# Performance work log

Measured on AMD Instinct MI355X. Metric: run time of the kernel, lower is better.

Reference implementation:

```python
import jax, jax.numpy as jnp
import numpy as np

NEG_SLOPE = 0.01  # torch F.leaky_relu default

def _lrelu(x):
    return jax.nn.leaky_relu(x, NEG_SLOPE)

def setup_inputs() -> dict:
    key = jax.random.key(0)
    ks = jax.random.split(key, 24)
    B, N, E = 512, 20000, 640000
    n_enc_1, n_enc_2, n_z = 512, 256, 64
    n_dec_2, n_dec_1, hidden = 256, 512, 256
    p = lambda k, shp, fan: jax.random.normal(k, shp, jnp.float32) * (1.0 / np.sqrt(fan))
    return {
        "data": jax.random.normal(ks[0], (B, N), jnp.float32),
        "noise": jax.random.normal(ks[1], (B, N), jnp.float32),
        "edge_index": jax.random.randint(ks[2], (2, E), 0, N, jnp.int32),
        "w_gcn": jax.random.normal(ks[3], (), jnp.float32),
        "b_gcn": jax.random.normal(ks[4], (), jnp.float32) * 0.1,
        "enc1_w": p(ks[5], (N, n_enc_1), N), "enc1_b": p(ks[6], (n_enc_1,), N),
        "enc2_w": p(ks[7], (n_enc_1, n_enc_2), n_enc_1), "enc2_b": p(ks[8], (n_enc_2,), n_enc_1),
        "enc3_w": p(ks[9], (n_enc_2, n_z), n_enc_2), "enc3_b": p(ks[10], (n_z,), n_enc_2),
        "dec1_w": p(ks[11], (n_z, n_dec_2), n_z), "dec1_b": p(ks[12], (n_dec_2,), n_z),
        "dec2_w": p(ks[13], (n_dec_2, n_dec_1), n_dec_2), "dec2_b": p(ks[14], (n_dec_1,), n_dec_2),
        "dec3_w": p(ks[15], (n_dec_1, N), n_dec_1), "dec3_b": p(ks[16], (N,), n_dec_1),
        "disc1_w": p(ks[17], (n_z, hidden), n_z), "disc1_b": p(ks[18], (hidden,), n_z),
        "disc2_w": p(ks[19], (hidden, hidden), hidden), "disc2_b": p(ks[20], (hidden,), hidden),
        "disc3_w": p(ks[21], (hidden, 1), hidden), "disc3_b": p(ks[22], (1,), hidden),
    }

def _gcn_batched(x, edge_index, w_gcn, b_gcn):
    # x: [B, N] -> GCNConv(1,1, improved=True) applied per row, vectorized.
    B, N = x.shape
    src, dst = edge_index[0], edge_index[1]
    loop = jnp.arange(N, dtype=src.dtype)
    src_a = jnp.concatenate([src, loop])
    dst_a = jnp.concatenate([dst, loop])
    # improved=True: self-loop edge weight 2.0
    ew = jnp.concatenate([jnp.ones(src.shape[0], x.dtype), jnp.full((N,), 2.0, x.dtype)])
    deg = jax.ops.segment_sum(ew, dst_a, num_segments=N)
    dinv = jnp.where(deg > 0, jax.lax.rsqrt(deg), 0.0)
    norm = dinv[src_a] * ew * dinv[dst_a]  # [E+N]
    xl = x * w_gcn                         # lin (1x1 weight, no bias)
    msgs = xl[:, src_a] * norm[None, :]    # [B, E+N]
    agg = jnp.zeros_like(x).at[:, dst_a].add(msgs)
    return agg + b_gcn

def reference(data, noise, edge_index, w_gcn, b_gcn,
              enc1_w, enc1_b, enc2_w, enc2_b, enc3_w, enc3_b,
              dec1_w, dec1_b, dec2_w, dec2_b, dec3_w, dec3_b,
              disc1_w, disc1_b, disc2_w, disc2_b, disc3_w, disc3_b):
    x = data + noise * 0.1
    gcn_out = _lrelu(_gcn_batched(x, edge_index, w_gcn, b_gcn))  # [B, N]
    h1 = _lrelu(gcn_out @ enc1_w + enc1_b)
    h2 = _lrelu(h1 @ enc2_w + enc2_b)
    z = _lrelu(h2 @ enc3_w + enc3_b)
    d1 = _lrelu(z @ dec1_w + dec1_b)
    d2 = _lrelu(d1 @ dec2_w + dec2_b)
    dec_h3 = _lrelu(d2 @ dec3_w + dec3_b)
    g1 = _lrelu(z @ disc1_w + disc1_b)
    g2 = _lrelu(g1 @ disc2_w + disc2_b)
    d = jax.nn.sigmoid(g2 @ disc3_w + disc3_b)
    return (dec_h3, z, d)
```

## Files before the change

kernel.cpp:

```cpp
#include <hip/hip_runtime.h>
#include <hip/hip_bf16.h>


#define LRELU(v) ((v) > 0.f ? (v) : 0.01f * (v))

static constexpr int Bb = 512;
static constexpr int Nn = 20000;
static constexpr int Ee = 640000;
static constexpr int KBn = 2500;
static constexpr int NPD = 20096;

typedef __attribute__((ext_vector_type(8))) short short8;
typedef __attribute__((ext_vector_type(4))) float f32x4;

__device__ __forceinline__ ushort f2bf(float f) {
  uint u = __builtin_bit_cast(uint, f);
  u = u + 0x7FFFu + ((u >> 16) & 1u);
  return (ushort)(u >> 16);
}
__device__ __forceinline__ float bfLo(uint u) {
  return __builtin_bit_cast(float, u << 16);
}
__device__ __forceinline__ float bfHi(uint u) {
  return __builtin_bit_cast(float, u & 0xffff0000u);
}

__global__ void transpose_xs_k(const float* __restrict__ a, const float* __restrict__ nz,
                               const float* __restrict__ dinv, ushort* __restrict__ xs) {
  __shared__ ushort tile[64][65];
  int c0 = blockIdx.x * 64;
  int p = blockIdx.y;
  int chunk = p >> 1;
  int sub = (p & 1) * 64;
  int rbase = p * 64;
  for (int i = threadIdx.x; i < 64 * 64; i += 256) {
    int rr = i >> 6, cc = i & 63;
    int r = rbase + rr, c = c0 + cc;
    ushort v = 0;
    if (c < Nn) {
      size_t idx = (size_t)r * Nn + c;
      v = f2bf(dinv[c] * (a[idx] + 0.1f * nz[idx]));
    }
    tile[rr][cc] = v;
  }
  __syncthreads();
  for (int i = threadIdx.x; i < 64 * 64; i += 256) {
    int cc = i >> 6, rr = i & 63;
    int c = c0 + cc;
    if (c < Nn) xs[(size_t)chunk * Nn * 128 + (size_t)c * 128 + sub + rr] = tile[rr][cc];
  }
}

__global__ void hist_check_k(const int* __restrict__ src, const int* __restrict__ dst, int E,
                             int* __restrict__ cnt, int* __restrict__ flag) {
  int i = blockIdx.x * 256 + threadIdx.x;
  if (i < E) {
    int s = src[i], d = dst[i];
    if ((unsigned)s >= (unsigned)Nn || (unsigned)d >= (unsigned)Nn) {
      atomicExch(flag, 1);
    } else {
      atomicAdd(&cnt[d], 1);
    }
  }
}

__global__ void offs_k(const int* __restrict__ cnt, int* __restrict__ offs,
                       int* __restrict__ cursor, float* __restrict__ dinv,
                       int* __restrict__ bump) {
  int i = blockIdx.x * 256 + threadIdx.x;
  int l = threadIdx.x & 63;
  int v = (i < Nn) ? cnt[i] : 0;
  int x = v;
#pragma unroll
  for (int d = 1; d < 64; d <<= 1) {
    int t = __shfl_up(x, d);
    if (l >= d) x += t;
  }
  int total = __shfl(x, 63);
  int base = 0;
  if (l == 0) base = atomicAdd(bump, total);
  base = __shfl(base, 0);
  int excl = base + x - v;
  if (i < Nn) {
    offs[i] = excl;
    cursor[i] = excl;
    dinv[i] = rsqrtf(2.0f + (float)v);
  }
}

__global__ void scatter_k(const int* __restrict__ src, const int* __restrict__ dst, int E,
                          int* __restrict__ cursor, uint* __restrict__ eOff) {
  int i = blockIdx.x * 256 + threadIdx.x;
  if (i < E) {
    int s = src[i], d = dst[i];
    if ((unsigned)s >= (unsigned)Nn || (unsigned)d >= (unsigned)Nn) return;
    int p = atomicAdd(&cursor[d], 1);
    eOff[p] = (uint)s * 256u;
  }
}

__global__ __launch_bounds__(256) void spmm_fm_k(
    const ushort* __restrict__ xs, const uint* __restrict__ eOff, const int* __restrict__ offs,
    const int* __restrict__ cnt, const float* __restrict__ dinv, const float* __restrict__ wg,
    const float* __restrict__ bg, ushort* __restrict__ gfm) {
  __shared__ uint sIdx[4][64];
  __shared__ ushort sOut[128][8];
  int bid = blockIdx.x;
  int chunk = bid & 3;
  int grp = bid >> 2;
  int wv = threadIdx.x >> 6, l = threadIdx.x & 63;
  const char* base = (const char*)(xs + (size_t)chunk * Nn * 128) + l * 4;
  float wgv = wg[0], bb = bg[0];

#pragma unroll
  for (int sub = 0; sub < 2; ++sub) {
    int n = grp * 8 + wv * 2 + sub;
    int o = offs[n], c = cnt[n];
    const uint* ep = eOff + o;
    uint su = *(const uint*)(base + (size_t)n * 256);
    float a00 = 2.0f * bfLo(su), a01 = 2.0f * bfHi(su);
    float a10 = 0.f, a11 = 0.f;

    for (int bi = 0; bi < c; bi += 64) {
      int rem = c - bi;
      if (rem > 64) rem = 64;
      sIdx[wv][l] = (l < rem) ? ep[bi + l] : 0u;
      int i = 0;
      for (; i + 8 <= rem; i += 8) {
        uint u[8];
#pragma unroll
        for (int j = 0; j < 8; ++j) u[j] = *(const uint*)(base + sIdx[wv][i + j]);
#pragma unroll
        for (int j = 0; j < 8; j += 2) {
          a00 += bfLo(u[j]);
          a01 += bfHi(u[j]);
          a10 += bfLo(u[j + 1]);
          a11 += bfHi(u[j + 1]);
        }
      }
      for (; i < rem; ++i) {
        uint u = *(const uint*)(base + sIdx[wv][i]);
        a00 += bfLo(u);
        a01 += bfHi(u);
      }
    }

    float wdn = wgv * dinv[n];
    float v0 = wdn * (a00 + a10) + bb;
    float v1 = wdn * (a01 + a11) + bb;
    v0 = LRELU(v0);
    v1 = LRELU(v1);
    int j = wv * 2 + sub;
    sOut[2 * l][j] = f2bf(v0);
    sOut[2 * l + 1][j] = f2bf(v1);
  }
  __syncthreads();
  int row = threadIdx.x >> 1, half = threadIdx.x & 1;
  uint2 v = *(const uint2*)&sOut[row][half * 4];
  int m = chunk * 128 + row;
  *(uint2*)&gfm[((size_t)grp * 512 + m) * 8 + half * 4] = v;
}

__global__ void conv_we_k(const float* __restrict__ W, ushort* __restrict__ wef) {
  int n = blockIdx.x * 256 + threadIdx.x;
  int kb = blockIdx.y;
  ushort v[8];
#pragma unroll
  for (int j = 0; j < 8; ++j) v[j] = f2bf(W[(size_t)(8 * kb + j) * 512 + n]);
  uint4 pk;
  pk.x = (uint)v[0] | ((uint)v[1] << 16);
  pk.y = (uint)v[2] | ((uint)v[3] << 16);
  pk.z = (uint)v[4] | ((uint)v[5] << 16);
  pk.w = (uint)v[6] | ((uint)v[7] << 16);
  *(uint4*)&wef[((size_t)kb * 512 + n) * 8] = pk;
}

__global__ __launch_bounds__(256) void fmg_enc1_k(const ushort* __restrict__ gfm,
                                                  const ushort* __restrict__ wef,
                                                  float* __restrict__ C) {
  int n0 = blockIdx.x * 128, m0 = blockIdx.y * 128;
  int l = threadIdx.x & 63, w = threadIdx.x >> 6;
  int wr = w >> 1, wc = w & 1;
  int lrow = l & 15, lkg = l >> 4;
  f32x4 acc[4][4] = {};
  int ksBeg = blockIdx.z * 25, ksEnd = ksBeg + 25;

  for (int ks = ksBeg; ks < ksEnd; ++ks) {
    int kb = ks * 4 + lkg;
    short8 a[4], b[4];
#pragma unroll
    for (int mi = 0; mi < 4; ++mi) {
      int m = m0 + wr * 64 + mi * 16 + lrow;
      a[mi] = *(const short8*)&gfm[((size_t)kb * 512 + m) * 8];
    }
#pragma unroll
    for (int nj = 0; nj < 4; ++nj) {
      int n = n0 + wc * 64 + nj * 16 + lrow;
      b[nj] = *(const short8*)&wef[((size_t)kb * 512 + n) * 8];
    }
#pragma unroll
    for (int mi = 0; mi < 4; ++mi)
#pragma unroll
      for (int nj = 0; nj < 4; ++nj)
        acc[mi][nj] = __builtin_amdgcn_mfma_f32_16x16x32_bf16(a[mi], b[nj], acc[mi][nj], 0, 0, 0);
  }

#pragma unroll
  for (int mi = 0; mi < 4; ++mi)
#pragma unroll
    for (int nj = 0; nj < 4; ++nj)
#pragma unroll
      for (int r = 0; r < 4; ++r) {
        int row = m0 + wr * 64 + mi * 16 + lkg * 4 + r;
        int col = n0 + wc * 64 + nj * 16 + lrow;
        atomicAdd(&C[(size_t)row * 512 + col], acc[mi][nj][r]);
      }
}

__global__ void conv_wf_k(const float* __restrict__ W, ushort* __restrict__ wf) {
  int n = blockIdx.x * 256 + threadIdx.x;
  int kb = blockIdx.y;
  if (n >= NPD) return;
  ushort v[8];
#pragma unroll
  for (int j = 0; j < 8; ++j)
    v[j] = (n < Nn) ? f2bf(W[(size_t)(8 * kb + j) * Nn + n]) : (ushort)0;
  uint4 pk;
  pk.x = (uint)v[0] | ((uint)v[1] << 16);
  pk.y = (uint)v[2] | ((uint)v[3] << 16);
  pk.z = (uint)v[4] | ((uint)v[5] << 16);
  pk.w = (uint)v[6] | ((uint)v[7] << 16);
  *(uint4*)&wf[((size_t)kb * NPD + n) * 8] = pk;
}

__global__ __launch_bounds__(256) void fmg_dec3_k(const ushort* __restrict__ d2f,
                                                  const ushort* __restrict__ wf,
                                                  const float* __restrict__ bias,
                                                  float* __restrict__ C) {
  int n0 = blockIdx.x * 128, m0 = blockIdx.y * 128;
  int l = threadIdx.x & 63, w = threadIdx.x >> 6;
  int wr = w >> 1, wc = w & 1;
  int lrow = l & 15, lkg = l >> 4;
  f32x4 acc[4][4] = {};

#pragma unroll 4
  for (int ks = 0; ks < 16; ++ks) {
    int kb = ks * 4 + lkg;
    short8 a[4], b[4];
#pragma unroll
    for (int mi = 0; mi < 4; ++mi) {
      int m = m0 + wr * 64 + mi * 16 + lrow;
      a[mi] = *(const short8*)&d2f[((size_t)kb * 512 + m) * 8];
    }
#pragma unroll
    for (int nj = 0; nj < 4; ++nj) {
      int n = n0 + wc * 64 + nj * 16 + lrow;
      b[nj] = *(const short8*)&wf[((size_t)kb * NPD + n) * 8];
    }
#pragma unroll
    for (int mi = 0; mi < 4; ++mi)
#pragma unroll
      for (int nj = 0; nj < 4; ++nj)
        acc[mi][nj] = __builtin_amdgcn_mfma_f32_16x16x32_bf16(a[mi], b[nj], acc[mi][nj], 0, 0, 0);
  }

#pragma unroll
  for (int mi = 0; mi < 4; ++mi)
#pragma unroll
    for (int nj = 0; nj < 4; ++nj)
#pragma unroll
      for (int r = 0; r < 4; ++r) {
        int row = m0 + wr * 64 + mi * 16 + lkg * 4 + r;
        int col = n0 + wc * 64 + nj * 16 + lrow;
        if (col < Nn) {
          float v = acc[mi][nj][r] + bias[col];
          C[(size_t)row * Nn + col] = LRELU(v);
        }
      }
}

__global__ __launch_bounds__(256) void tail2_k(
    const float* __restrict__ h1, const float* __restrict__ c1, const float* __restrict__ W2,
    const float* __restrict__ c2, const float* __restrict__ W3, const float* __restrict__ c3,
    const float* __restrict__ Wd1, const float* __restrict__ cd1, const float* __restrict__ Wd2,
    const float* __restrict__ cd2, const float* __restrict__ Wg1, const float* __restrict__ cg1,
    const float* __restrict__ Wg2, const float* __restrict__ cg2, const float* __restrict__ Wg3,
    const float* __restrict__ cg3, float* __restrict__ out_z, float* __restrict__ out_d,
    ushort* __restrict__ d2f) {
  __shared__ float s_h1[512];
  __shared__ float s_h2[256];
  __shared__ float s_z[64];
  __shared__ float s_d1[256];
  __shared__ float s_g1[256];
  __shared__ float s_g2[256];
  __shared__ float s_part[4][256];
  __shared__ float s_red[4];
  int rl = blockIdx.x;
  int t = threadIdx.x;
  int w = t >> 6, l = t & 63;

  {
    float r0 = h1[(size_t)rl * 512 + t] + c1[t];
    float r1 = h1[(size_t)rl * 512 + t + 256] + c1[t + 256];
    s_h1[t] = LRELU(r0);
    s_h1[t + 256] = LRELU(r1);
  }
  __syncthreads();

  {
    int c4 = l * 4;
    float a0 = 0.f, a1 = 0.f, a2 = 0.f, a3 = 0.f;
#pragma unroll 8
    for (int k = w * 128; k < w * 128 + 128; ++k) {
      float4 wv = *(const float4*)&W2[(size_t)k * 256 + c4];
      float x = s_h1[k];
      a0 += x * wv.x; a1 += x * wv.y; a2 += x * wv.z; a3 += x * wv.w;
    }
    float4 pv = {a0, a1, a2, a3};
    *(float4*)&s_part[w][c4] = pv;
  }
  __syncthreads();
  s_h2[t] = LRELU(s_part[0][t] + s_part[1][t] + s_part[2][t] + s_part[3][t] + c2[t]);
  __syncthreads();

  {
    int c = t >> 2, p = t & 3;
    float a = 0.f;
#pragma unroll 8
    for (int k = p * 64; k < p * 64 + 64; ++k) a += s_h2[k] * W3[(size_t)k * 64 + c];
    s_part[p][c] = a;
  }
  __syncthreads();
  if (t < 64) {
    float v = s_part[0][t] + s_part[1][t] + s_part[2][t] + s_part[3][t] + c3[t];
    v = LRELU(v);
    s_z[t] = v;
    out_z[(size_t)rl * 64 + t] = v;
  }
  __syncthreads();

  {
    float a = 0.f;
#pragma unroll
    for (int k = 0; k < 64; ++k) a += s_z[k] * Wd1[(size_t)k * 256 + t];
    s_d1[t] = LRELU(a + cd1[t]);
  }
  {
    float a = 0.f;
#pragma unroll
    for (int k = 0; k < 64; ++k) a += s_z[k] * Wg1[(size_t)k * 256 + t];
    s_g1[t] = LRELU(a + cg1[t]);
  }
  __syncthreads();

  {
    int g = t & 127, p = t >> 7;
    int c4 = g * 4;
    float a0 = 0.f, a1 = 0.f, a2 = 0.f, a3 = 0.f;
#pragma unroll 8
    for (int k = p * 128; k < p * 128 + 128; ++k) {
      float4 wv = *(const float4*)&Wd2[(size_t)k * 512 + c4];
      float x = s_d1[k];
      a0 += x * wv.x; a1 += x * wv.y; a2 += x * wv.z; a3 += x * wv.w;
    }
    float* sp = &s_part[0][0];
    float4 pv = {a0, a1, a2, a3};
    *(float4*)&sp[p * 512 + c4] = pv;
  }
  __syncthreads();
  {
    const float* sp = &s_part[0][0];
#pragma unroll
    for (int cc = 0; cc < 2; ++cc) {
      int c = t + cc * 256;
      float v = sp[c] + sp[512 + c] + cd2[c];
      v = LRELU(v);
      d2f[((size_t)(c >> 3) * 512 + rl) * 8 + (c & 7)] = f2bf(v);
    }
  }
  __syncthreads();

  {
    int c4 = l * 4;
    float a0 = 0.f, a1 = 0.f, a2 = 0.f, a3 = 0.f;
#pragma unroll 8
    for (int k = w * 64; k < w * 64 + 64; ++k) {
      float4 wv = *(const float4*)&Wg2[(size_t)k * 256 + c4];
      float x = s_g1[k];
      a0 += x * wv.x; a1 += x * wv.y; a2 += x * wv.z; a3 += x * wv.w;
    }
    float4 pv = {a0, a1, a2, a3};
    *(float4*)&s_part[w][c4] = pv;
  }
  __syncthreads();
  s_g2[t] = LRELU(s_part[0][t] + s_part[1][t] + s_part[2][t] + s_part[3][t] + cg2[t]);
  __syncthreads();

  {
    float p = s_g2[t] * Wg3[t];
#pragma unroll
    for (int o = 32; o > 0; o >>= 1) p += __shfl_down(p, o);
    if ((t & 63) == 0) s_red[t >> 6] = p;
    __syncthreads();
    if (t == 0) {
      float s = s_red[0] + s_red[1] + s_red[2] + s_red[3] + cg3[0];
      out_d[rl] = 1.f / (1.f + __expf(-s));
    }
  }
}

__global__ void sentinel_k(float* out, float val) { out[0] = val; }
__global__ void flag_sentinel_k(float* out, const int* flag) {
  if (*flag != 0) out[0] = 70000.0f;
}

extern "C" void kernel_launch(void* const* d_in, const int* in_sizes, int n_in,
                              void* d_out, int out_size, void* d_ws, size_t ws_size,
                              hipStream_t stream) {
  const float* data = (const float*)d_in[0];
  const float* noise = (const float*)d_in[1];
  const int* edge = (const int*)d_in[2];
  const int* esrc_in = edge;
  const int* edst_in = edge + Ee;
  const float* w_gcn = (const float*)d_in[3];
  const float* b_gcn = (const float*)d_in[4];
  const float* enc1_w = (const float*)d_in[5];
  const float* enc1_b = (const float*)d_in[6];
  const float* enc2_w = (const float*)d_in[7];
  const float* enc2_b = (const float*)d_in[8];
  const float* enc3_w = (const float*)d_in[9];
  const float* enc3_b = (const float*)d_in[10];
  const float* dec1_w = (const float*)d_in[11];
  const float* dec1_b = (const float*)d_in[12];
  const float* dec2_w = (const float*)d_in[13];
  const float* dec2_b = (const float*)d_in[14];
  const float* dec3_w = (const float*)d_in[15];
  const float* dec3_b = (const float*)d_in[16];
  const float* disc1_w = (const float*)d_in[17];
  const float* disc1_b = (const float*)d_in[18];
  const float* disc2_w = (const float*)d_in[19];
  const float* disc2_b = (const float*)d_in[20];
  const float* disc3_w = (const float*)d_in[21];
  const float* disc3_b = (const float*)d_in[22];

  char* w = (char*)d_ws;
  size_t o = 0;
  auto alloc = [&](size_t bytes) {
    size_t r = o;
    o = (o + bytes + 15) & ~(size_t)15;
    return r;
  };
  size_t r1 = alloc((size_t)64 * NPD * 8 * 2);
  ushort* xs = (ushort*)(w + r1);
  ushort* wef = (ushort*)(w + r1);
  ushort* wf = (ushort*)(w + r1);
  ushort* gfm = (ushort*)(w + alloc((size_t)KBn * 512 * 8 * 2));
  float* h1 = (float*)(w + alloc(512 * 512 * 4));
  ushort* d2f = (ushort*)(w + alloc((size_t)64 * 512 * 8 * 2));
  float* dinv = (float*)(w + alloc(Nn * 4));
  int* cnt = (int*)(w + alloc(Nn * 4));
  int* offs = (int*)(w + alloc(Nn * 4));
  int* cursor = (int*)(w + alloc(Nn * 4));
  uint* eOff = (uint*)(w + alloc(Ee * 4));
  int* flag = (int*)(w + alloc(16));

  float* outp = (float*)d_out;
  float* out_dec = outp;
  float* out_z = outp + (size_t)Bb * Nn;
  float* out_d = out_z + (size_t)Bb * 64;

  static const int expect_sizes[23] = {
      10240000, 10240000, 1280000, 1, 1,
      10240000, 512, 131072, 256, 16384, 64,
      16384, 256, 131072, 512, 10240000, 20000,
      16384, 256, 65536, 256, 256, 1};
  float host_sentinel = 0.f;
  if (n_in != 23) host_sentinel = 50000.f;
  else if (out_size != 10273280) host_sentinel = 80000.f;
  else if (ws_size < 46100000u) host_sentinel = 60000.f;
  else {
    for (int i = 0; i < 23; ++i)
      if (in_sizes[i] != expect_sizes[i]) { host_sentinel = 100000.f + 1000.f * i; break; }
  }

  hipMemsetAsync(cnt, 0, Nn * sizeof(int), stream);
  hipMemsetAsync(flag, 0, 2 * sizeof(int), stream);
  hist_check_k<<<(Ee + 255) / 256, 256, 0, stream>>>(esrc_in, edst_in, Ee, cnt, flag);
  offs_k<<<(Nn + 255) / 256, 256, 0, stream>>>(cnt, offs, cursor, dinv, flag + 1);
  scatter_k<<<(Ee + 255) / 256, 256, 0, stream>>>(esrc_in, edst_in, Ee, cursor, eOff);

  {
    dim3 g((Nn + 63) / 64, 8);
    transpose_xs_k<<<g, 256, 0, stream>>>(data, noise, dinv, xs);
  }
  spmm_fm_k<<<(Nn / 8) * 4, 256, 0, stream>>>(xs, eOff, offs, cnt, dinv, w_gcn, b_gcn, gfm);
  {
    dim3 g(2, KBn);
    conv_we_k<<<g, 256, 0, stream>>>(enc1_w, wef);
  }
  hipMemsetAsync(h1, 0, 512 * 512 * 4, stream);
  {
    dim3 g(512 / 128, 512 / 128, 25);
    fmg_enc1_k<<<g, 256, 0, stream>>>(gfm, wef, h1);
  }
  tail2_k<<<Bb, 256, 0, stream>>>(h1, enc1_b, enc2_w, enc2_b, enc3_w, enc3_b, dec1_w, dec1_b,
                                  dec2_w, dec2_b, disc1_w, disc1_b, disc2_w, disc2_b, disc3_w,
                                  disc3_b, out_z, out_d, d2f);
  {
    dim3 g((NPD + 255) / 256, 64);
    conv_wf_k<<<g, 256, 0, stream>>>(dec3_w, wf);
  }
  {
    dim3 g(NPD / 128, 512 / 128);
    fmg_dec3_k<<<g, 256, 0, stream>>>(d2f, wf, dec3_b, out_dec);
  }

  flag_sentinel_k<<<1, 1, 0, stream>>>(out_dec, flag);
  if (host_sentinel != 0.f) sentinel_k<<<1, 1, 0, stream>>>(out_dec, host_sentinel);
}
```

Measured before the change: 288.9 us.

## Split tail MLP kernel into encoder and parallel decoder/discriminator kernels

Splits the per-row tail MLP into two kernels. One computes the encoder layers down to z and writes z to a workspace buffer. The second launches twice as many blocks so the decoder and discriminator branches run in parallel. The change also widens the SpMM gather unroll from 8 to 16 with a new 4-wide remainder loop, raises the tail loop unroll factors, and moves the h1 memset earlier. It adds a kernel launch and a small global round trip for z in exchange for more block-level parallelism.

```diff
diff --git a/kernel.cpp b/kernel.cpp
--- a/kernel.cpp
+++ b/kernel.cpp
@@ -126,17 +126,31 @@
       if (rem > 64) rem = 64;
       sIdx[wv][l] = (l < rem) ? ep[bi + l] : 0u;
       int i = 0;
-      for (; i + 8 <= rem; i += 8) {
-        uint u[8];
-#pragma unroll
-        for (int j = 0; j < 8; ++j) u[j] = *(const uint*)(base + sIdx[wv][i + j]);
-#pragma unroll
-        for (int j = 0; j < 8; j += 2) {
+      for (; i + 16 <= rem; i += 16) {
+        uint u[16];
+#pragma unroll
+        for (int j = 0; j < 16; ++j) u[j] = *(const uint*)(base + sIdx[wv][i + j]);
+#pragma unroll
+        for (int j = 0; j < 16; j += 2) {
           a00 += bfLo(u[j]);
           a01 += bfHi(u[j]);
           a10 += bfLo(u[j + 1]);
           a11 += bfHi(u[j + 1]);
         }
+      }
+      for (; i + 4 <= rem; i += 4) {
+        uint u0 = *(const uint*)(base + sIdx[wv][i]);
+        uint u1 = *(const uint*)(base + sIdx[wv][i + 1]);
+        uint u2 = *(const uint*)(base + sIdx[wv][i + 2]);
+        uint u3 = *(const uint*)(base + sIdx[wv][i + 3]);
+        a00 += bfLo(u0);
+        a01 += bfHi(u0);
+        a10 += bfLo(u1);
+        a11 += bfHi(u1);
+        a00 += bfLo(u2);
+        a01 += bfHi(u2);
+        a10 += bfLo(u3);
+        a11 += bfHi(u3);
       }
       for (; i < rem; ++i) {
         uint u = *(const uint*)(base + sIdx[wv][i]);
@@ -279,22 +293,17 @@
       }
 }
 
-__global__ __launch_bounds__(256) void tail2_k(
-    const float* __restrict__ h1, const float* __restrict__ c1, const float* __restrict__ W2,
-    const float* __restrict__ c2, const float* __restrict__ W3, const float* __restrict__ c3,
-    const float* __restrict__ Wd1, const float* __restrict__ cd1, const float* __restrict__ Wd2,
-    const float* __restrict__ cd2, const float* __restrict__ Wg1, const float* __restrict__ cg1,
-    const float* __restrict__ Wg2, const float* __restrict__ cg2, const float* __restrict__ Wg3,
-    const float* __restrict__ cg3, float* __restrict__ out_z, float* __restrict__ out_d,
-    ushort* __restrict__ d2f) {
+__global__ __launch_bounds__(256) void tailA_k(const float* __restrict__ h1,
+                                               const float* __restrict__ c1,
+                                               const float* __restrict__ W2,
+                                               const float* __restrict__ c2,
+                                               const float* __restrict__ W3,
+                                               const float* __restrict__ c3,
+                                               float* __restrict__ zbuf,
+                                               float* __restrict__ out_z) {
   __shared__ float s_h1[512];
   __shared__ float s_h2[256];
-  __shared__ float s_z[64];
-  __shared__ float s_d1[256];
-  __shared__ float s_g1[256];
-  __shared__ float s_g2[256];
   __shared__ float s_part[4][256];
-  __shared__ float s_red[4];
   int rl = blockIdx.x;
   int t = threadIdx.x;
   int w = t >> 6, l = t & 63;
@@ -310,7 +319,7 @@
   {
     int c4 = l * 4;
     float a0 = 0.f, a1 = 0.f, a2 = 0.f, a3 = 0.f;
-#pragma unroll 8
+#pragma unroll 16
     for (int k = w * 128; k < w * 128 + 128; ++k) {
       float4 wv = *(const float4*)&W2[(size_t)k * 256 + c4];
       float x = s_h1[k];
@@ -326,7 +335,7 @@
   {
     int c = t >> 2, p = t & 3;
     float a = 0.f;
-#pragma unroll 8
+#pragma unroll 16
     for (int k = p * 64; k < p * 64 + 64; ++k) a += s_h2[k] * W3[(size_t)k * 64 + c];
     s_part[p][c] = a;
   }
@@ -334,77 +343,96 @@
   if (t < 64) {
     float v = s_part[0][t] + s_part[1][t] + s_part[2][t] + s_part[3][t] + c3[t];
     v = LRELU(v);
-    s_z[t] = v;
+    zbuf[(size_t)rl * 64 + t] = v;
     out_z[(size_t)rl * 64 + t] = v;
   }
-  __syncthreads();
-
-  {
-    float a = 0.f;
-#pragma unroll
-    for (int k = 0; k < 64; ++k) a += s_z[k] * Wd1[(size_t)k * 256 + t];
-    s_d1[t] = LRELU(a + cd1[t]);
-  }
-  {
-    float a = 0.f;
-#pragma unroll
-    for (int k = 0; k < 64; ++k) a += s_z[k] * Wg1[(size_t)k * 256 + t];
-    s_g1[t] = LRELU(a + cg1[t]);
-  }
-  __syncthreads();
-
-  {
-    int g = t & 127, p = t >> 7;
-    int c4 = g * 4;
-    float a0 = 0.f, a1 = 0.f, a2 = 0.f, a3 = 0.f;
-#pragma unroll 8
-    for (int k = p * 128; k < p * 128 + 128; ++k) {
-      float4 wv = *(const float4*)&Wd2[(size_t)k * 512 + c4];
-      float x = s_d1[k];
-      a0 += x * wv.x; a1 += x * wv.y; a2 += x * wv.z; a3 += x * wv.w;
-    }
-    float* sp = &s_part[0][0];
-    float4 pv = {a0, a1, a2, a3};
-    *(float4*)&sp[p * 512 + c4] = pv;
-  }
-  __syncthreads();
-  {
-    const float* sp = &s_part[0][0];
-#pragma unroll
-    for (int cc = 0; cc < 2; ++cc) {
-      int c = t + cc * 256;
-      float v = sp[c] + sp[512 + c] + cd2[c];
-      v = LRELU(v);
-      d2f[((size_t)(c >> 3) * 512 + rl) * 8 + (c & 7)] = f2bf(v);
-    }
-  }
-  __syncthreads();
-
-  {
-    int c4 = l * 4;
-    float a0 = 0.f, a1 = 0.f, a2 = 0.f, a3 = 0.f;
-#pragma unroll 8
-    for (int k = w * 64; k < w * 64 + 64; ++k) {
-      float4 wv = *(const float4*)&Wg2[(size_t)k * 256 + c4];
-      float x = s_g1[k];
-      a0 += x * wv.x; a1 += x * wv.y; a2 += x * wv.z; a3 += x * wv.w;
-    }
-    float4 pv = {a0, a1, a2, a3};
-    *(float4*)&s_part[w][c4] = pv;
-  }
-  __syncthreads();
-  s_g2[t] = LRELU(s_part[0][t] + s_part[1][t] + s_part[2][t] + s_part[3][t] + cg2[t]);
-  __syncthreads();
-
-  {
-    float p = s_g2[t] * Wg3[t];
-#pragma unroll
-    for (int o = 32; o > 0; o >>= 1) p += __shfl_down(p, o);
-    if ((t & 63) == 0) s_red[t >> 6] = p;
+}
+
+__global__ __launch_bounds__(256) void tailB_k(
+    const float* __restrict__ zbuf, const float* __restrict__ Wd1, const float* __restrict__ cd1,
+    const float* __restrict__ Wd2, const float* __restrict__ cd2, const float* __restrict__ Wg1,
+    const float* __restrict__ cg1, const float* __restrict__ Wg2, const float* __restrict__ cg2,
+    const float* __restrict__ Wg3, const float* __restrict__ cg3, float* __restrict__ out_d,
+    ushort* __restrict__ d2f) {
+  __shared__ float s_z[64];
+  __shared__ float s_x[256];
+  __shared__ float s_part[4][256];
+  __shared__ float s_g2[256];
+  __shared__ float s_red[4];
+  int bid = blockIdx.x;
+  int rl = bid & 511;
+  int t = threadIdx.x;
+  int w = t >> 6, l = t & 63;
+
+  if (t < 64) s_z[t] = zbuf[(size_t)rl * 64 + t];
+  __syncthreads();
+
+  if (bid < 512) {
+    {
+      float a = 0.f;
+#pragma unroll
+      for (int k = 0; k < 64; ++k) a += s_z[k] * Wd1[(size_t)k * 256 + t];
+      s_x[t] = LRELU(a + cd1[t]);
+    }
     __syncthreads();
-    if (t == 0) {
-      float s = s_red[0] + s_red[1] + s_red[2] + s_red[3] + cg3[0];
-      out_d[rl] = 1.f / (1.f + __expf(-s));
+    {
+      int g = t & 127, p = t >> 7;
+      int c4 = g * 4;
+      float a0 = 0.f, a1 = 0.f, a2 = 0.f, a3 = 0.f;
+#pragma unroll 16
+      for (int k = p * 128; k < p * 128 + 128; ++k) {
+        float4 wv = *(const float4*)&Wd2[(size_t)k * 512 + c4];
+        float x = s_x[k];
+        a0 += x * wv.x; a1 += x * wv.y; a2 += x * wv.z; a3 += x * wv.w;
+      }
+      float* sp = &s_part[0][0];
+      float4 pv = {a0, a1, a2, a3};
+      *(float4*)&sp[p * 512 + c4] = pv;
+    }
+    __syncthreads();
+    {
+      const float* sp = &s_part[0][0];
+#pragma unroll
+      for (int cc = 0; cc < 2; ++cc) {
+        int c = t + cc * 256;
+        float v = sp[c] + sp[512 + c] + cd2[c];
+        v = LRELU(v);
+        d2f[((size_t)(c >> 3) * 512 + rl) * 8 + (c & 7)] = f2bf(v);
+      }
+    }
+  } else {
+    {
+      float a = 0.f;
+#pragma unroll
+      for (int k = 0; k < 64; ++k) a += s_z[k] * Wg1[(size_t)k * 256 + t];
+      s_x[t] = LRELU(a + cg1[t]);
+    }
+    __syncthreads();
+    {
+      int c4 = l * 4;
+      float a0 = 0.f, a1 = 0.f, a2 = 0.f, a3 = 0.f;
+#pragma unroll 16
+      for (int k = w * 64; k < w * 64 + 64; ++k) {
+        float4 wv = *(const float4*)&Wg2[(size_t)k * 256 + c4];
+        float x = s_x[k];
+        a0 += x * wv.x; a1 += x * wv.y; a2 += x * wv.z; a3 += x * wv.w;
+      }
+      float4 pv = {a0, a1, a2, a3};
+      *(float4*)&s_part[w][c4] = pv;
+    }
+    __syncthreads();
+    s_g2[t] = LRELU(s_part[0][t] + s_part[1][t] + s_part[2][t] + s_part[3][t] + cg2[t]);
+    __syncthreads();
+    {
+      float p = s_g2[t] * Wg3[t];
+#pragma unroll
+      for (int o = 32; o > 0; o >>= 1) p += __shfl_down(p, o);
+      if ((t & 63) == 0) s_red[t >> 6] = p;
+      __syncthreads();
+      if (t == 0) {
+        float s = s_red[0] + s_red[1] + s_red[2] + s_red[3] + cg3[0];
+        out_d[rl] = 1.f / (1.f + __expf(-s));
+      }
     }
   }
 }
@@ -457,6 +485,7 @@
   ushort* gfm = (ushort*)(w + alloc((size_t)KBn * 512 * 8 * 2));
   float* h1 = (float*)(w + alloc(512 * 512 * 4));
   ushort* d2f = (ushort*)(w + alloc((size_t)64 * 512 * 8 * 2));
+  float* zbuf = (float*)(w + alloc((size_t)512 * 64 * 4));
   float* dinv = (float*)(w + alloc(Nn * 4));
   int* cnt = (int*)(w + alloc(Nn * 4));
   int* offs = (int*)(w + alloc(Nn * 4));
@@ -485,6 +514,7 @@
 
   hipMemsetAsync(cnt, 0, Nn * sizeof(int), stream);
   hipMemsetAsync(flag, 0, 2 * sizeof(int), stream);
+  hipMemsetAsync(h1, 0, 512 * 512 * 4, stream);
   hist_check_k<<<(Ee + 255) / 256, 256, 0, stream>>>(esrc_in, edst_in, Ee, cnt, flag);
   offs_k<<<(Nn + 255) / 256, 256, 0, stream>>>(cnt, offs, cursor, dinv, flag + 1);
   scatter_k<<<(Ee + 255) / 256, 256, 0, stream>>>(esrc_in, edst_in, Ee, cursor, eOff);
@@ -498,14 +528,13 @@
     dim3 g(2, KBn);
     conv_we_k<<<g, 256, 0, stream>>>(enc1_w, wef);
   }
-  hipMemsetAsync(h1, 0, 512 * 512 * 4, stream);
   {
     dim3 g(512 / 128, 512 / 128, 25);
     fmg_enc1_k<<<g, 256, 0, stream>>>(gfm, wef, h1);
   }
-  tail2_k<<<Bb, 256, 0, stream>>>(h1, enc1_b, enc2_w, enc2_b, enc3_w, enc3_b, dec1_w, dec1_b,
-                                  dec2_w, dec2_b, disc1_w, disc1_b, disc2_w, disc2_b, disc3_w,
-                                  disc3_b, out_z, out_d, d2f);
+  tailA_k<<<Bb, 256, 0, stream>>>(h1, enc1_b, enc2_w, enc2_b, enc3_w, enc3_b, zbuf, out_z);
+  tailB_k<<<2 * Bb, 256, 0, stream>>>(zbuf, dec1_w, dec1_b, dec2_w, dec2_b, disc1_w, disc1_b,
+                                      disc2_w, disc2_b, disc3_w, disc3_b, out_d, d2f);
   {
     dim3 g((NPD + 255) / 256, 64);
     conv_wf_k<<<g, 256, 0, stream>>>(dec3_w, wf);
```

Result: no change. 284.5 us (-1.5%).
